# Kernel optimization log

Measured on AMD Instinct MI355X. Metric: run time of the kernel, lower is better.

The kernel has to match this reference:

```python
import jax, jax.numpy as jnp
import numpy as np

B, Q, K, DQ, DK, H, DV = 4, 512, 512, 512, 512, 256, 512


def setup_inputs() -> dict:
    key = jax.random.key(0)
    ks = jax.random.split(key, 9)
    return {
        "query": jax.random.normal(ks[0], (B, Q, DQ), dtype=jnp.float32),
        "key": jax.random.normal(ks[1], (B, K, DK), dtype=jnp.float32),
        "value": jax.random.normal(ks[2], (B, K, DV), dtype=jnp.float32),
        "Wq": jax.random.normal(ks[3], (DQ, H), dtype=jnp.float32) / np.sqrt(DQ),
        "bq": jax.random.normal(ks[4], (H,), dtype=jnp.float32) * 0.01,
        "Wk": jax.random.normal(ks[5], (DK, H), dtype=jnp.float32) / np.sqrt(DK),
        "bk": jax.random.normal(ks[6], (H,), dtype=jnp.float32) * 0.01,
        "wv": jax.random.normal(ks[7], (H,), dtype=jnp.float32) / np.sqrt(H),
        "bv": jax.random.normal(ks[8], (), dtype=jnp.float32) * 0.01,
    }


def reference(query, key, value, Wq, bq, Wk, bk, wv, bv):
    # Projections: [B,Q,H] and [B,K,H]
    q = jnp.einsum("bqd,dh->bqh", query, Wq) + bq
    k = jnp.einsum("bkd,dh->bkh", key, Wk) + bk
    # Broadcast add + tanh: [B,Q,K,H] (the large intermediate)
    feat = jnp.tanh(q[:, :, None, :] + k[:, None, :, :])
    # Linear-to-scalar score: [B,Q,K]
    score = jnp.einsum("bqkh,h->bqk", feat, wv) + bv
    attention_weight = jax.nn.softmax(score, axis=-1)
    # Dropout is identity at eval; weighted sum over keys: [B,Q,DV]
    context = jnp.einsum("bqk,bkd->bqd", attention_weight, value)
    return (context, attention_weight)
```

## Files before the change

### kernel.cpp

```cpp
#include <hip/hip_runtime.h>
#include <hip/hip_bf16.h>

#define B_ 4
#define Q_ 512
#define K_ 512
#define DQ_ 512
#define H_ 256
#define DV_ 512

#define SC2 2.8853900817779268f

typedef unsigned short u16;
typedef short bf16x8 __attribute__((ext_vector_type(8)));
typedef float f32x4 __attribute__((ext_vector_type(4)));
typedef float f32x2 __attribute__((ext_vector_type(2)));
typedef unsigned short u16x4 __attribute__((ext_vector_type(4)));

__device__ __forceinline__ unsigned bsplit(float a) {
    unsigned u  = __float_as_uint(a);
    unsigned hi = (u + 0x7FFFu + ((u >> 16) & 1u)) >> 16;
    float hf = __uint_as_float(hi << 16);
    float l  = a - hf;
    unsigned ul = __float_as_uint(l);
    unsigned lo = (ul + 0x7FFFu + ((ul >> 16) & 1u)) >> 16;
    return (hi << 16) | lo;
}

__device__ __forceinline__ void gld16(const void* g, void* l) {
    __builtin_amdgcn_global_load_lds(
        (const __attribute__((address_space(1))) unsigned int*)g,
        (__attribute__((address_space(3))) unsigned int*)l, 16, 0, 0);
}

__device__ __forceinline__ void pair_acc(
    f32x2 Eq0, f32x2 Eq1, float ek0, float ek1,
    float w0, float w1, float w01, f32x2& acc)
{
    f32x2 e0 = Eq0 * (f32x2){ek0, ek0};
    f32x2 e1 = Eq1 * (f32x2){ek1, ek1};
    f32x2 s  = e0 + e1;
    f32x2 den = __builtin_elementwise_fma(e0, e1, s);
    den = den + (f32x2){1.f, 1.f};
    f32x2 num = __builtin_elementwise_fma(e1, (f32x2){w0, w0}, (f32x2){w01, w01});
    num = __builtin_elementwise_fma(e0, (f32x2){w1, w1}, num);
    f32x2 r = {__builtin_amdgcn_rcpf(den.x), __builtin_amdgcn_rcpf(den.y)};
    acc = __builtin_elementwise_fma(num, r, acc);
}

__global__ __launch_bounds__(256) void prep_all(
    const float* __restrict__ query, const float* __restrict__ key,
    const float* __restrict__ Wq, const float* __restrict__ Wk,
    const float* __restrict__ value,
    u16* __restrict__ qA_hi, u16* __restrict__ qA_lo,
    u16* __restrict__ WT_hi, u16* __restrict__ WT_lo,
    u16* __restrict__ vT_hi, u16* __restrict__ vT_lo)
{
    const int bx  = blockIdx.x;
    const int tid = threadIdx.x;

    if (bx < 2048) {
        const int z = bx >> 10;
        const float* src = z ? key : query;
        u16* dh = qA_hi + (long long)z * 1048576;
        u16* dl = qA_lo + (long long)z * 1048576;
        long long i4 = (long long)(bx & 1023) * 256 + tid;
        float4 v = ((const float4*)src)[i4];
        unsigned a = bsplit(v.x), b = bsplit(v.y), c = bsplit(v.z), d = bsplit(v.w);
        u16x4 h4 = {(u16)(a >> 16), (u16)(b >> 16), (u16)(c >> 16), (u16)(d >> 16)};
        u16x4 l4 = {(u16)(a & 0xFFFF), (u16)(b & 0xFFFF), (u16)(c & 0xFFFF), (u16)(d & 0xFFFF)};
        *(u16x4*)(dh + i4 * 4) = h4;
        *(u16x4*)(dl + i4 * 4) = l4;
        return;
    }

    __shared__ float t[32][33];
    const int flat = bx - 2048;
    const int z  = flat >> 8;
    const int rem = flat & 255;
    const int gx = rem & 15, gy = rem >> 4;
    const int x = tid & 31, y = tid >> 5;
    const float* src; u16 *dh, *dl; int C;
    if (z < 2) {
        if (gy >= 8) return;
        src = z ? Wk : Wq; C = 256;
        dh = WT_hi + (long long)z * 131072;
        dl = WT_lo + (long long)z * 131072;
    } else {
        src = value + (long long)(z - 2) * 262144; C = 512;
        dh = vT_hi + (long long)(z - 2) * 262144;
        dl = vT_lo + (long long)(z - 2) * 262144;
    }
    const int r0 = gx * 32, c0 = gy * 32;
    #pragma unroll
    for (int i = 0; i < 32; i += 8)
        t[y + i][x] = src[(long long)(r0 + y + i) * C + c0 + x];
    __syncthreads();
    {
        const int r = tid >> 3, c = tid & 7;
        unsigned p0 = bsplit(t[4 * c + 0][r]);
        unsigned p1 = bsplit(t[4 * c + 1][r]);
        unsigned p2 = bsplit(t[4 * c + 2][r]);
        unsigned p3 = bsplit(t[4 * c + 3][r]);
        long long o = (long long)(c0 + r) * 512 + r0 + 4 * c;
        u16x4 h4 = {(u16)(p0 >> 16), (u16)(p1 >> 16), (u16)(p2 >> 16), (u16)(p3 >> 16)};
        u16x4 l4 = {(u16)(p0 & 0xFFFF), (u16)(p1 & 0xFFFF), (u16)(p2 & 0xFFFF), (u16)(p3 & 0xFFFF)};
        *(u16x4*)(dh + o) = h4;
        *(u16x4*)(dl + o) = l4;
    }
}

__global__ __launch_bounds__(256) void mfma_gemm(
    const u16* __restrict__ Ah0, const u16* __restrict__ Al0,
    const u16* __restrict__ Bh0, const u16* __restrict__ Bl0,
    const float* __restrict__ biasq, const float* __restrict__ biask,
    float* __restrict__ outp, int mode, int Kd,
    long long sA, long long sB, long long sO)
{
    const int z = blockIdx.z;
    const u16* Ah = Ah0 + z * sA;
    const u16* Al = Al0 + z * sA;
    const u16* Bh = Bh0 + z * sB;
    const u16* Bl = Bl0 + z * sB;

    const int m0 = blockIdx.x * 64;
    const int n0 = blockIdx.y * 64;

    __shared__ u16 AhS[64 * 64], AlS[64 * 64], BhS[64 * 64], BlS[64 * 64];

    const int tid = threadIdx.x;
    const int lane = tid & 63, w = tid >> 6;
    const int wr = w >> 1, wc = w & 1;
    const int lrow = lane & 15, lgrp = lane >> 4;

    f32x4 acc[2][2] = {};

    for (int k0 = 0; k0 < Kd; k0 += 64) {
        #pragma unroll
        for (int it = 0; it < 2; ++it) {
            int idx = tid + it * 256;
            int row = idx >> 3, u = idx & 7;
            long long go = (long long)(m0 + row) * Kd + k0 + ((u ^ (row & 7)) << 3);
            long long gb = (long long)(n0 + row) * Kd + k0 + ((u ^ (row & 7)) << 3);
            gld16(Ah + go, AhS + idx * 8);
            gld16(Al + go, AlS + idx * 8);
            gld16(Bh + gb, BhS + idx * 8);
            gld16(Bl + gb, BlS + idx * 8);
        }
        __syncthreads();

        #pragma unroll
        for (int kk = 0; kk < 2; ++kk) {
            bf16x8 ah[2], al[2], bh[2], bl[2];
            #pragma unroll
            for (int f = 0; f < 2; ++f) {
                int ar = wr * 32 + f * 16 + lrow;
                int au = (kk * 4 + lgrp) ^ (ar & 7);
                ah[f] = *(const bf16x8*)(AhS + ar * 64 + au * 8);
                al[f] = *(const bf16x8*)(AlS + ar * 64 + au * 8);
                int br = wc * 32 + f * 16 + lrow;
                int bu = (kk * 4 + lgrp) ^ (br & 7);
                bh[f] = *(const bf16x8*)(BhS + br * 64 + bu * 8);
                bl[f] = *(const bf16x8*)(BlS + br * 64 + bu * 8);
            }
            #pragma unroll
            for (int fm = 0; fm < 2; ++fm)
                #pragma unroll
                for (int fn = 0; fn < 2; ++fn) {
                    acc[fm][fn] = __builtin_amdgcn_mfma_f32_16x16x32_bf16(ah[fm], bh[fn], acc[fm][fn], 0, 0, 0);
                    acc[fm][fn] = __builtin_amdgcn_mfma_f32_16x16x32_bf16(ah[fm], bl[fn], acc[fm][fn], 0, 0, 0);
                    acc[fm][fn] = __builtin_amdgcn_mfma_f32_16x16x32_bf16(al[fm], bh[fn], acc[fm][fn], 0, 0, 0);
                }
        }
        __syncthreads();
    }

    if (mode == 0) {
        const float* bs = z ? biask : biasq;
        #pragma unroll
        for (int fm = 0; fm < 2; ++fm)
            #pragma unroll
            for (int fn = 0; fn < 2; ++fn)
                #pragma unroll
                for (int r = 0; r < 4; ++r) {
                    int m = m0 + wr * 32 + fm * 16 + lgrp * 4 + r;
                    int n = n0 + wc * 32 + fn * 16 + lrow;
                    float v = __builtin_amdgcn_exp2f((acc[fm][fn][r] + bs[n]) * SC2);
                    if (z == 0) {
                        outp[(((long long)(m >> 2) * H_ + n) << 2) + (m & 3)] = v;
                    } else {
                        int bb = m >> 9, k = m & 511;
                        outp[sO + (((long long)(bb * 64 + (n >> 2)) * 512 + k) << 2) + (n & 3)] = v;
                    }
                }
    } else {
        float* C = outp + (long long)z * sO;
        #pragma unroll
        for (int fm = 0; fm < 2; ++fm)
            #pragma unroll
            for (int fn = 0; fn < 2; ++fn)
                #pragma unroll
                for (int r = 0; r < 4; ++r) {
                    int m = m0 + wr * 32 + fm * 16 + lgrp * 4 + r;
                    int n = n0 + wc * 32 + fn * 16 + lrow;
                    C[(long long)m * DV_ + n] = acc[fm][fn][r];
                }
    }
}

#define QT 4

__global__ __launch_bounds__(1024, 8) void score_softmax(
    const float* __restrict__ qp4E,
    const float* __restrict__ kT4E,
    const float* __restrict__ wv,
    float* __restrict__ attn_out,
    u16* __restrict__ aB_hi, u16* __restrict__ aB_lo)
{
    const int b   = blockIdx.y;
    const int q0  = blockIdx.x * QT;
    const int tid = threadIdx.x;
    const int k16 = tid & 255;
    const int qtr = tid >> 8;
    const int lane = tid & 63;

    __shared__ float lq[H_][QT];
    __shared__ float lwp[H_ / 2][4];
    __shared__ float pacc[3][2][256][4];
    __shared__ float red[4][QT];

    if (tid < H_) {
        const float4* qsrc = (const float4*)qp4E + ((long long)(b * (Q_ / 4) + blockIdx.x)) * H_;
        *(float4*)&lq[tid][0] = qsrc[tid];
    } else if (tid < H_ + H_ / 2) {
        int p = tid - H_;
        float w0 = wv[2 * p], w1 = wv[2 * p + 1];
        lwp[p][0] = w0; lwp[p][1] = w1; lwp[p][2] = w0 + w1; lwp[p][3] = 0.f;
    }
    __syncthreads();

    f32x2 a01[2] = {{0.f,0.f},{0.f,0.f}}, a23[2] = {{0.f,0.f},{0.f,0.f}};
    const float4* kvec = (const float4*)kT4E + (long long)b * (H_ / 4) * K_ + k16;
    const int g0 = qtr * 16;

    float4 kA = kvec[(long long)g0 * K_];
    float4 kB = kvec[(long long)g0 * K_ + 256];
    #pragma unroll 2
    for (int gi = 0; gi < 16; ++gi) {
        const int g = g0 + gi;
        float4 kAc = kA, kBc = kB;
        if (gi < 15) {
            kA = kvec[(long long)(g + 1) * K_];
            kB = kvec[(long long)(g + 1) * K_ + 256];
        }
        float4 q4_0 = *(const float4*)&lq[(g << 2) + 0][0];
        float4 q4_1 = *(const float4*)&lq[(g << 2) + 1][0];
        float4 q4_2 = *(const float4*)&lq[(g << 2) + 2][0];
        float4 q4_3 = *(const float4*)&lq[(g << 2) + 3][0];
        float4 wp0 = *(const float4*)&lwp[(g << 1) + 0][0];
        float4 wp1 = *(const float4*)&lwp[(g << 1) + 1][0];

        f32x2 q0_01 = {q4_0.x, q4_0.y}, q0_23 = {q4_0.z, q4_0.w};
        f32x2 q1_01 = {q4_1.x, q4_1.y}, q1_23 = {q4_1.z, q4_1.w};
        f32x2 q2_01 = {q4_2.x, q4_2.y}, q2_23 = {q4_2.z, q4_2.w};
        f32x2 q3_01 = {q4_3.x, q4_3.y}, q3_23 = {q4_3.z, q4_3.w};

        pair_acc(q0_01, q1_01, kAc.x, kAc.y, wp0.x, wp0.y, wp0.z, a01[0]);
        pair_acc(q0_23, q1_23, kAc.x, kAc.y, wp0.x, wp0.y, wp0.z, a23[0]);
        pair_acc(q2_01, q3_01, kAc.z, kAc.w, wp1.x, wp1.y, wp1.z, a01[0]);
        pair_acc(q2_23, q3_23, kAc.z, kAc.w, wp1.x, wp1.y, wp1.z, a23[0]);
        pair_acc(q0_01, q1_01, kBc.x, kBc.y, wp0.x, wp0.y, wp0.z, a01[1]);
        pair_acc(q0_23, q1_23, kBc.x, kBc.y, wp0.x, wp0.y, wp0.z, a23[1]);
        pair_acc(q2_01, q3_01, kBc.z, kBc.w, wp1.x, wp1.y, wp1.z, a01[1]);
        pair_acc(q2_23, q3_23, kBc.z, kBc.w, wp1.x, wp1.y, wp1.z, a23[1]);
    }

    if (qtr) {
        #pragma unroll
        for (int kk = 0; kk < 2; ++kk) {
            float4 v = make_float4(a01[kk].x, a01[kk].y, a23[kk].x, a23[kk].y);
            *(float4*)&pacc[qtr - 1][kk][k16][0] = v;
        }
    }
    __syncthreads();

    float e[2][QT];
    if (!qtr) {
        #pragma unroll
        for (int kk = 0; kk < 2; ++kk) {
            float4 t0 = *(const float4*)&pacc[0][kk][k16][0];
            float4 t1 = *(const float4*)&pacc[1][kk][k16][0];
            float4 t2 = *(const float4*)&pacc[2][kk][k16][0];
            float at0 = a01[kk].x + t0.x + t1.x + t2.x;
            float at1 = a01[kk].y + t0.y + t1.y + t2.y;
            float at2 = a23[kk].x + t0.z + t1.z + t2.z;
            float at3 = a23[kk].y + t0.w + t1.w + t2.w;
            e[kk][0] = __builtin_amdgcn_exp2f(-SC2 * at0);
            e[kk][1] = __builtin_amdgcn_exp2f(-SC2 * at1);
            e[kk][2] = __builtin_amdgcn_exp2f(-SC2 * at2);
            e[kk][3] = __builtin_amdgcn_exp2f(-SC2 * at3);
        }
        #pragma unroll
        for (int qq = 0; qq < QT; ++qq) {
            float v = e[0][qq] + e[1][qq];
            #pragma unroll
            for (int off = 32; off; off >>= 1) v += __shfl_xor(v, off);
            if (lane == 0) red[tid >> 6][qq] = v;
        }
    }
    __syncthreads();
    if (!qtr) {
        #pragma unroll
        for (int qq = 0; qq < QT; ++qq) {
            float v = red[0][qq] + red[1][qq] + red[2][qq] + red[3][qq];
            float rv = __builtin_amdgcn_rcpf(v);
            #pragma unroll
            for (int kk = 0; kk < 2; ++kk) {
                float a = e[kk][qq] * rv;
                long long o = (long long)(b * Q_ + q0 + qq) * K_ + k16 + kk * 256;
                attn_out[o] = a;
                unsigned p = bsplit(a);
                aB_hi[o] = (u16)(p >> 16);
                aB_lo[o] = (u16)(p & 0xFFFF);
            }
        }
    }
}

extern "C" void kernel_launch(void* const* d_in, const int* in_sizes, int n_in,
                              void* d_out, int out_size, void* d_ws, size_t ws_size,
                              hipStream_t stream) {
    const float* query = (const float*)d_in[0];
    const float* key   = (const float*)d_in[1];
    const float* value = (const float*)d_in[2];
    const float* Wq    = (const float*)d_in[3];
    const float* bq    = (const float*)d_in[4];
    const float* Wk    = (const float*)d_in[5];
    const float* bk    = (const float*)d_in[6];
    const float* wv    = (const float*)d_in[7];

    float* out = (float*)d_out;
    float* ctx_out  = out;
    float* attn_out = out + (size_t)B_ * Q_ * DV_;

    float* ws   = (float*)d_ws;
    float* qp4  = ws;
    float* kT4  = qp4 + 524288;
    u16* qA_hi  = (u16*)(kT4 + 524288);
    u16* kA_hi  = qA_hi + 1048576;
    u16* qA_lo  = kA_hi + 1048576;
    u16* kA_lo  = qA_lo + 1048576;
    u16* WqT_hi = kA_lo + 1048576;
    u16* WkT_hi = WqT_hi + 131072;
    u16* WqT_lo = WkT_hi + 131072;
    u16* WkT_lo = WqT_lo + 131072;
    u16* vT_hi  = WkT_lo + 131072;
    u16* vT_lo  = vT_hi + 1048576;
    u16* aB_hi  = vT_lo + 1048576;
    u16* aB_lo  = aB_hi + 1048576;
    (void)qA_lo; (void)WqT_lo; (void)n_in; (void)ws_size; (void)in_sizes; (void)out_size;

    hipLaunchKernelGGL(prep_all, dim3(3584), dim3(256), 0, stream,
                       query, key, Wq, Wk, value,
                       qA_hi, qA_lo, WqT_hi, WqT_lo, vT_hi, vT_lo);

    hipLaunchKernelGGL(mfma_gemm, dim3(32, 4, 2), dim3(256), 0, stream,
                       qA_hi, qA_lo, WqT_hi, WqT_lo, bq, bk, qp4, 0, 512,
                       (long long)1048576, (long long)131072, (long long)524288);

    hipLaunchKernelGGL(score_softmax, dim3(Q_ / QT, B_), dim3(1024), 0, stream,
                       qp4, kT4, wv, attn_out, aB_hi, aB_lo);

    hipLaunchKernelGGL(mfma_gemm, dim3(8, 8, 4), dim3(256), 0, stream,
                       aB_hi, aB_lo, vT_hi, vT_lo, (const float*)nullptr, (const float*)nullptr,
                       ctx_out, 2, 512,
                       (long long)262144, (long long)262144, (long long)262144);
}
```

Before: 67.04 us.

## Remap score_softmax threads to split H eight ways with four keys each

Changes the score kernel's work split. Instead of four quarter-groups of 256 threads, each covering two keys over 16 H-groups, it uses eight groups of 128 threads, each covering four keys over 8 H-groups. The cross-group reduction now has all threads write partials to a larger shared buffer, and 512 threads sum them and run the softmax. The explicit next-iteration prefetch of K and the minimum-blocks launch hint are dropped. This balances the final reduction and softmax work across more threads, at the cost of much more shared memory (about 64KB of partials), which may limit occupancy, and the loss of the software prefetch.

```diff
diff --git a/kernel.cpp b/kernel.cpp
--- a/kernel.cpp
+++ b/kernel.cpp
@@ -209,7 +209,7 @@
 
 #define QT 4
 
-__global__ __launch_bounds__(1024, 8) void score_softmax(
+__global__ __launch_bounds__(1024) void score_softmax(
     const float* __restrict__ qp4E,
     const float* __restrict__ kT4E,
     const float* __restrict__ wv,
@@ -219,14 +219,13 @@
     const int b   = blockIdx.y;
     const int q0  = blockIdx.x * QT;
     const int tid = threadIdx.x;
-    const int k16 = tid & 255;
-    const int qtr = tid >> 8;
-    const int lane = tid & 63;
+    const int k7  = tid & 127;
+    const int oct = tid >> 7;
 
     __shared__ float lq[H_][QT];
     __shared__ float lwp[H_ / 2][4];
-    __shared__ float pacc[3][2][256][4];
-    __shared__ float red[4][QT];
+    __shared__ float pacc[8][128][16];
+    __shared__ float red[8][QT];
 
     if (tid < H_) {
         const float4* qsrc = (const float4*)qp4E + ((long long)(b * (Q_ / 4) + blockIdx.x)) * H_;
@@ -238,20 +237,18 @@
     }
     __syncthreads();
 
-    f32x2 a01[2] = {{0.f,0.f},{0.f,0.f}}, a23[2] = {{0.f,0.f},{0.f,0.f}};
-    const float4* kvec = (const float4*)kT4E + (long long)b * (H_ / 4) * K_ + k16;
-    const int g0 = qtr * 16;
-
-    float4 kA = kvec[(long long)g0 * K_];
-    float4 kB = kvec[(long long)g0 * K_ + 256];
+    f32x2 a01[4] = {{0.f,0.f},{0.f,0.f},{0.f,0.f},{0.f,0.f}};
+    f32x2 a23[4] = {{0.f,0.f},{0.f,0.f},{0.f,0.f},{0.f,0.f}};
+    const float4* kvec = (const float4*)kT4E + (long long)b * (H_ / 4) * K_ + k7;
+    const int g0 = oct * 8;
+
     #pragma unroll 2
-    for (int gi = 0; gi < 16; ++gi) {
+    for (int gi = 0; gi < 8; ++gi) {
         const int g = g0 + gi;
-        float4 kAc = kA, kBc = kB;
-        if (gi < 15) {
-            kA = kvec[(long long)(g + 1) * K_];
-            kB = kvec[(long long)(g + 1) * K_ + 256];
-        }
+        float4 kv0 = kvec[(long long)g * K_];
+        float4 kv1 = kvec[(long long)g * K_ + 128];
+        float4 kv2 = kvec[(long long)g * K_ + 256];
+        float4 kv3 = kvec[(long long)g * K_ + 384];
         float4 q4_0 = *(const float4*)&lq[(g << 2) + 0][0];
         float4 q4_1 = *(const float4*)&lq[(g << 2) + 1][0];
         float4 q4_2 = *(const float4*)&lq[(g << 2) + 2][0];
@@ -264,64 +261,68 @@
         f32x2 q2_01 = {q4_2.x, q4_2.y}, q2_23 = {q4_2.z, q4_2.w};
         f32x2 q3_01 = {q4_3.x, q4_3.y}, q3_23 = {q4_3.z, q4_3.w};
 
-        pair_acc(q0_01, q1_01, kAc.x, kAc.y, wp0.x, wp0.y, wp0.z, a01[0]);
-        pair_acc(q0_23, q1_23, kAc.x, kAc.y, wp0.x, wp0.y, wp0.z, a23[0]);
-        pair_acc(q2_01, q3_01, kAc.z, kAc.w, wp1.x, wp1.y, wp1.z, a01[0]);
-        pair_acc(q2_23, q3_23, kAc.z, kAc.w, wp1.x, wp1.y, wp1.z, a23[0]);
-        pair_acc(q0_01, q1_01, kBc.x, kBc.y, wp0.x, wp0.y, wp0.z, a01[1]);
-        pair_acc(q0_23, q1_23, kBc.x, kBc.y, wp0.x, wp0.y, wp0.z, a23[1]);
-        pair_acc(q2_01, q3_01, kBc.z, kBc.w, wp1.x, wp1.y, wp1.z, a01[1]);
-        pair_acc(q2_23, q3_23, kBc.z, kBc.w, wp1.x, wp1.y, wp1.z, a23[1]);
-    }
-
-    if (qtr) {
-        #pragma unroll
-        for (int kk = 0; kk < 2; ++kk) {
-            float4 v = make_float4(a01[kk].x, a01[kk].y, a23[kk].x, a23[kk].y);
-            *(float4*)&pacc[qtr - 1][kk][k16][0] = v;
-        }
+        pair_acc(q0_01, q1_01, kv0.x, kv0.y, wp0.x, wp0.y, wp0.z, a01[0]);
+        pair_acc(q0_23, q1_23, kv0.x, kv0.y, wp0.x, wp0.y, wp0.z, a23[0]);
+        pair_acc(q2_01, q3_01, kv0.z, kv0.w, wp1.x, wp1.y, wp1.z, a01[0]);
+        pair_acc(q2_23, q3_23, kv0.z, kv0.w, wp1.x, wp1.y, wp1.z, a23[0]);
+
+        pair_acc(q0_01, q1_01, kv1.x, kv1.y, wp0.x, wp0.y, wp0.z, a01[1]);
+        pair_acc(q0_23, q1_23, kv1.x, kv1.y, wp0.x, wp0.y, wp0.z, a23[1]);
+        pair_acc(q2_01, q3_01, kv1.z, kv1.w, wp1.x, wp1.y, wp1.z, a01[1]);
+        pair_acc(q2_23, q3_23, kv1.z, kv1.w, wp1.x, wp1.y, wp1.z, a23[1]);
+
+        pair_acc(q0_01, q1_01, kv2.x, kv2.y, wp0.x, wp0.y, wp0.z, a01[2]);
+        pair_acc(q0_23, q1_23, kv2.x, kv2.y, wp0.x, wp0.y, wp0.z, a23[2]);
+        pair_acc(q2_01, q3_01, kv2.z, kv2.w, wp1.x, wp1.y, wp1.z, a01[2]);
+        pair_acc(q2_23, q3_23, kv2.z, kv2.w, wp1.x, wp1.y, wp1.z, a23[2]);
+
+        pair_acc(q0_01, q1_01, kv3.x, kv3.y, wp0.x, wp0.y, wp0.z, a01[3]);
+        pair_acc(q0_23, q1_23, kv3.x, kv3.y, wp0.x, wp0.y, wp0.z, a23[3]);
+        pair_acc(q2_01, q3_01, kv3.z, kv3.w, wp1.x, wp1.y, wp1.z, a01[3]);
+        pair_acc(q2_23, q3_23, kv3.z, kv3.w, wp1.x, wp1.y, wp1.z, a23[3]);
+    }
+
+    #pragma unroll
+    for (int kk = 0; kk < 4; ++kk) {
+        float4 v = make_float4(a01[kk].x, a01[kk].y, a23[kk].x, a23[kk].y);
+        *(float4*)&pacc[oct][k7][kk * 4] = v;
     }
     __syncthreads();
 
-    float e[2][QT];
-    if (!qtr) {
-        #pragma unroll
-        for (int kk = 0; kk < 2; ++kk) {
-            float4 t0 = *(const float4*)&pacc[0][kk][k16][0];
-            float4 t1 = *(const float4*)&pacc[1][kk][k16][0];
-            float4 t2 = *(const float4*)&pacc[2][kk][k16][0];
-            float at0 = a01[kk].x + t0.x + t1.x + t2.x;
-            float at1 = a01[kk].y + t0.y + t1.y + t2.y;
-            float at2 = a23[kk].x + t0.z + t1.z + t2.z;
-            float at3 = a23[kk].y + t0.w + t1.w + t2.w;
-            e[kk][0] = __builtin_amdgcn_exp2f(-SC2 * at0);
-            e[kk][1] = __builtin_amdgcn_exp2f(-SC2 * at1);
-            e[kk][2] = __builtin_amdgcn_exp2f(-SC2 * at2);
-            e[kk][3] = __builtin_amdgcn_exp2f(-SC2 * at3);
-        }
+    float ee[QT];
+    if (tid < 512) {
+        const int k7e = tid & 127, kke = tid >> 7;
+        float4 s = make_float4(0.f, 0.f, 0.f, 0.f);
+        #pragma unroll
+        for (int o = 0; o < 8; ++o) {
+            float4 t = *(const float4*)&pacc[o][k7e][kke * 4];
+            s.x += t.x; s.y += t.y; s.z += t.z; s.w += t.w;
+        }
+        ee[0] = __builtin_amdgcn_exp2f(-SC2 * s.x);
+        ee[1] = __builtin_amdgcn_exp2f(-SC2 * s.y);
+        ee[2] = __builtin_amdgcn_exp2f(-SC2 * s.z);
+        ee[3] = __builtin_amdgcn_exp2f(-SC2 * s.w);
         #pragma unroll
         for (int qq = 0; qq < QT; ++qq) {
-            float v = e[0][qq] + e[1][qq];
+            float v = ee[qq];
             #pragma unroll
             for (int off = 32; off; off >>= 1) v += __shfl_xor(v, off);
-            if (lane == 0) red[tid >> 6][qq] = v;
+            if ((tid & 63) == 0) red[tid >> 6][qq] = v;
         }
     }
     __syncthreads();
-    if (!qtr) {
+    if (tid < 512) {
+        const int k7e = tid & 127, kke = tid >> 7;
         #pragma unroll
         for (int qq = 0; qq < QT; ++qq) {
-            float v = red[0][qq] + red[1][qq] + red[2][qq] + red[3][qq];
-            float rv = __builtin_amdgcn_rcpf(v);
-            #pragma unroll
-            for (int kk = 0; kk < 2; ++kk) {
-                float a = e[kk][qq] * rv;
-                long long o = (long long)(b * Q_ + q0 + qq) * K_ + k16 + kk * 256;
-                attn_out[o] = a;
-                unsigned p = bsplit(a);
-                aB_hi[o] = (u16)(p >> 16);
-                aB_lo[o] = (u16)(p & 0xFFFF);
-            }
+            float tot = red[0][qq] + red[1][qq] + red[2][qq] + red[3][qq]
+                      + red[4][qq] + red[5][qq] + red[6][qq] + red[7][qq];
+            float a = ee[qq] * __builtin_amdgcn_rcpf(tot);
+            long long o = (long long)(b * Q_ + q0 + qq) * K_ + k7e + kke * 128;
+            attn_out[o] = a;
+            unsigned p = bsplit(a);
+            aB_hi[o] = (u16)(p >> 16);
+            aB_lo[o] = (u16)(p & 0xFFFF);
         }
     }
 }
```

Measured after the change: 68.28 us. No clear change (+1.9%).
